# Optimization experiments

Measured on AMD Instinct MI355X. Metric: run time of the kernel, lower is better.

Reference implementation:

```python
import jax, jax.numpy as jnp
import numpy as np

B, I, H = 512, 256, 512
UNFOLDS = 6


def setup_inputs() -> dict:
    key = jax.random.key(0)
    ks = jax.random.split(key, 13)
    u = lambda k, shape, lo, hi: jax.random.uniform(k, shape, jnp.float32, lo, hi)
    sensory_erev = (2.0 * jax.random.randint(ks[3], (I, H), 0, 2) - 1.0).astype(jnp.float32)
    erev = (2.0 * jax.random.randint(ks[7], (H, H), 0, 2) - 1.0).astype(jnp.float32)
    return {
        "inputs": jax.random.normal(ks[0], (B, I), jnp.float32),
        "state": jax.random.normal(ks[1], (B, H), jnp.float32),
        "sensory_mu": u(ks[2], (I, H), 0.3, 0.8),
        "sensory_sigma": u(ks[4], (I, H), 3.0, 8.0),
        "sensory_W": u(ks[5], (I, H), 0.01, 1.0),
        "sensory_erev": sensory_erev,
        "mu": u(ks[6], (H, H), 0.3, 0.8),
        "sigma": u(ks[8], (H, H), 3.0, 8.0),
        "W": u(ks[9], (H, H), 0.01, 1.0),
        "erev": erev,
        "vleak": u(ks[10], (H,), -0.2, 0.2),
        "gleak": jnp.ones((H,), jnp.float32),
        "cm": jnp.full((H,), 0.5, jnp.float32),
    }


def reference(inputs, state, sensory_mu, sensory_sigma, sensory_W, sensory_erev,
              mu, sigma, W, erev, vleak, gleak, cm):
    # Sensory synapse currents (computed once): (B, I, H) broadcast
    sensory_act = jax.nn.sigmoid((inputs[:, :, None] - sensory_mu[None]) * sensory_sigma[None])
    sensory_w_act = sensory_W[None] * sensory_act                      # (B, I, H)
    w_num_sensory = jnp.sum(sensory_w_act * sensory_erev[None], axis=1)  # (B, H)
    w_den_sensory = jnp.sum(sensory_w_act, axis=1)                        # (B, H)

    def step(v_pre, _):
        # recurrent synapse gating: (B, H_pre, H_post)
        act = jax.nn.sigmoid((v_pre[:, :, None] - mu[None]) * sigma[None])
        w_act = W[None] * act
        w_num = jnp.sum(w_act * erev[None], axis=1) + w_num_sensory
        w_den = jnp.sum(w_act, axis=1) + w_den_sensory
        numerator = cm * v_pre + gleak * vleak + w_num
        denominator = cm + gleak + w_den
        return numerator / (denominator + 1e-8), None

    v_pre, _ = jax.lax.scan(step, state, None, length=UNFOLDS)
    return v_pre
```

## Files before the change

kernel.cpp:

```cpp
#include <hip/hip_runtime.h>

#define LTC_B 512
#define LTC_H 512
#define LTC_I 256

static constexpr float kL2E = 1.4426950408889634f;

struct alignas(16) HPair { _Float16 a0, a1, c0, c1, wz0, wz1, wd0, wd1; };

typedef unsigned int u32;
#define AS_G __attribute__((address_space(1)))
#define AS_L __attribute__((address_space(3)))

__device__ __forceinline__ void ldg_lds16(const void* g, void* l) {
    __builtin_amdgcn_global_load_lds((const AS_G u32*)g, (AS_L u32*)l, 16, 0, 0);
}

template<int K>
__global__ void ltc_prep(const float* __restrict__ mu, const float* __restrict__ sigma,
                         const float* __restrict__ W, const float* __restrict__ erev,
                         HPair* __restrict__ slab) {
    const int t = blockIdx.x * 256 + threadIdx.x;
    if (t >= K * 256) return;
    const int hh   = t & 63;
    const int rest = t >> 6;
    const int jp   = rest & (K / 2 - 1);
    const int ht   = rest / (K / 2);
    const int h    = ht * 64 + hh;
    const int g0   = (2 * jp) * LTC_H + h;
    const int g1   = g0 + LTC_H;
    HPair o;
    o.a0 = (_Float16)(-sigma[g0] * kL2E);
    o.a1 = (_Float16)(-sigma[g1] * kL2E);
    o.c0 = (_Float16)(mu[g0] * sigma[g0] * kL2E);
    o.c1 = (_Float16)(mu[g1] * sigma[g1] * kL2E);
    o.wz0 = (_Float16)(W[g0] * erev[g0]);
    o.wz1 = (_Float16)(W[g1] * erev[g1]);
    o.wd0 = (_Float16)(W[g0]);
    o.wd1 = (_Float16)(W[g1]);
    slab[t] = o;
}

template<int K, bool RECUR>
__global__ __launch_bounds__(256, 4)
void ltc_pass(const float* __restrict__ vsrc,
              const HPair* __restrict__ slab,
              const float* __restrict__ snum, const float* __restrict__ sden,
              const float* __restrict__ vleak, const float* __restrict__ gleak,
              const float* __restrict__ cm,
              float* __restrict__ onum, float* __restrict__ oden,
              float* __restrict__ vout)
{
    __shared__ HPair wbuf[2][16 * 64];
    const int tid  = threadIdx.x;
    const int lane = tid & 63;
    const int wu   = __builtin_amdgcn_readfirstlane(tid >> 6);
    const int ht   = blockIdx.x;
    const int b    = blockIdx.y * 4 + wu;
    const float* __restrict__ vrow = vsrc + (size_t)b * K;

    constexpr int NC = K / 32;
    const int rot = (int)((blockIdx.x + 7u * blockIdx.y) & (NC - 1));
    const char* slabt = (const char*)slab + (size_t)ht * (K * 512);

    {
        const char* src = slabt + rot * 16384 + wu * 4096;
        char* dst = (char*)&wbuf[0][0] + wu * 4096;
        #pragma unroll
        for (int rr = 0; rr < 4; ++rr)
            ldg_lds16(src + rr * 1024 + lane * 16, dst + rr * 1024);
    }

    float na = 0.f, da = 0.f;

    #pragma unroll
    for (int i = 0; i < NC; ++i) {
        const int c = (rot + i) & (NC - 1);
        __syncthreads();
        if (i + 1 < NC) {
            const int cn = (rot + i + 1) & (NC - 1);
            const char* src = slabt + cn * 16384 + wu * 4096;
            char* dst = (char*)&wbuf[(i + 1) & 1][0] + wu * 4096;
            #pragma unroll
            for (int rr = 0; rr < 4; ++rr)
                ldg_lds16(src + rr * 1024 + lane * 16, dst + rr * 1024);
        }
        const HPair* wb = &wbuf[i & 1][0];
        const float* __restrict__ vch = vrow + c * 32;

        HPair pr[16];
        #pragma unroll
        for (int jj = 0; jj < 16; ++jj) pr[jj] = wb[jj * 64 + lane];

        #pragma unroll
        for (int jj = 0; jj < 16; ++jj) {
            const float vj0 = vch[2 * jj];
            const float vj1 = vch[2 * jj + 1];
            const float t0 = fmaf((float)pr[jj].a0, vj0, (float)pr[jj].c0);
            const float t1 = fmaf((float)pr[jj].a1, vj1, (float)pr[jj].c1);
            const float e0 = __builtin_amdgcn_exp2f(t0);
            const float e1 = __builtin_amdgcn_exp2f(t1);
            const float d0 = 1.0f + e0;
            const float d1 = 1.0f + e1;
            const float rr = __builtin_amdgcn_rcpf(d0 * d1);
            const float s0 = rr * d1;
            const float s1 = rr * d0;
            na = fmaf((float)pr[jj].wz0, s0, na);
            da = fmaf((float)pr[jj].wd0, s0, da);
            na = fmaf((float)pr[jj].wz1, s1, na);
            da = fmaf((float)pr[jj].wd1, s1, da);
        }
    }

    const int h  = ht * 64 + lane;
    const int bh = b * LTC_H + h;
    if constexpr (RECUR) {
        const float gl = gleak[h], vl = vleak[h], c0 = cm[h];
        const float vp = vsrc[bh];
        const float num = fmaf(c0, vp, gl * vl) + na + snum[bh];
        const float den = c0 + gl + da + sden[bh];
        vout[bh] = num * __builtin_amdgcn_rcpf(den + 1e-8f);
    } else {
        onum[bh] = na;
        oden[bh] = da;
    }
}

extern "C" void kernel_launch(void* const* d_in, const int* in_sizes, int n_in,
                              void* d_out, int out_size, void* d_ws, size_t ws_size,
                              hipStream_t stream) {
    const float* inputs = (const float*)d_in[0];
    const float* state  = (const float*)d_in[1];
    const float* smu    = (const float*)d_in[2];
    const float* ssig   = (const float*)d_in[3];
    const float* sW     = (const float*)d_in[4];
    const float* serev  = (const float*)d_in[5];
    const float* mu     = (const float*)d_in[6];
    const float* sig    = (const float*)d_in[7];
    const float* W      = (const float*)d_in[8];
    const float* erev   = (const float*)d_in[9];
    const float* vleak  = (const float*)d_in[10];
    const float* gleak  = (const float*)d_in[11];
    const float* cm     = (const float*)d_in[12];

    float* out  = (float*)d_out;
    char*  ws   = (char*)d_ws;
    float* snum = (float*)(ws);
    float* sden = (float*)(ws + 1 * 1048576);
    float* vA   = (float*)(ws + 2 * 1048576);
    HPair* rslab = (HPair*)(ws + 3 * 1048576);
    HPair* sslab = (HPair*)(ws + 5 * 1048576);

    ltc_prep<LTC_H><<<LTC_H * 256 / 256, 256, 0, stream>>>(mu, sig, W, erev, rslab);
    ltc_prep<LTC_I><<<LTC_I * 256 / 256, 256, 0, stream>>>(smu, ssig, sW, serev, sslab);

    dim3 grid(LTC_H / 64, LTC_B / 4);
    dim3 blk(256);

    ltc_pass<LTC_I, false><<<grid, blk, 0, stream>>>(
        inputs, sslab, nullptr, nullptr, nullptr, nullptr, nullptr,
        snum, sden, nullptr);

    const float* vin = state;
    float* targets[6] = {vA, out, vA, out, vA, out};
    for (int s = 0; s < 6; ++s) {
        ltc_pass<LTC_H, true><<<grid, blk, 0, stream>>>(
            vin, rslab, snum, sden, vleak, gleak, cm,
            nullptr, nullptr, targets[s]);
        vin = targets[s];
    }
}
```

Baseline: 334.4 us.

## Split weight slab into fp32 gate coefficients and fp16 weights using fdot2

Splits the per-synapse slab into a float4 array of fp32 sigmoid coefficients and a separate fp16 weight pair array, each double-buffered in LDS with smaller 16-row chunks. The sigmoid pair is packed to fp16 and both accumulations use a packed fp16 dot2 instruction. The per-block chunk rotation is removed, and the previous-state load now reads from the already offset row. This cuts the fp16-to-fp32 conversions and FMA count, but raises global and LDS traffic for the coefficients and adds fp16 rounding of the activations.

Measured after the change: 346.5 us. 3.6% more time.

```diff
diff --git a/kernel.cpp b/kernel.cpp
--- a/kernel.cpp
+++ b/kernel.cpp
@@ -6,9 +6,12 @@
 
 static constexpr float kL2E = 1.4426950408889634f;
 
-struct alignas(16) HPair { _Float16 a0, a1, c0, c1, wz0, wz1, wd0, wd1; };
+typedef _Float16 half2v __attribute__((ext_vector_type(2)));
+typedef __fp16   fp16x2 __attribute__((ext_vector_type(2)));
+typedef unsigned int u32;
 
-typedef unsigned int u32;
+struct alignas(8) WPair { half2v wz, wd; };
+
 #define AS_G __attribute__((address_space(1)))
 #define AS_L __attribute__((address_space(3)))
 
@@ -19,7 +22,7 @@
 template<int K>
 __global__ void ltc_prep(const float* __restrict__ mu, const float* __restrict__ sigma,
                          const float* __restrict__ W, const float* __restrict__ erev,
-                         HPair* __restrict__ slab) {
+                         float4* __restrict__ acs, WPair* __restrict__ wps) {
     const int t = blockIdx.x * 256 + threadIdx.x;
     if (t >= K * 256) return;
     const int hh   = t & 63;
@@ -29,29 +32,33 @@
     const int h    = ht * 64 + hh;
     const int g0   = (2 * jp) * LTC_H + h;
     const int g1   = g0 + LTC_H;
-    HPair o;
-    o.a0 = (_Float16)(-sigma[g0] * kL2E);
-    o.a1 = (_Float16)(-sigma[g1] * kL2E);
-    o.c0 = (_Float16)(mu[g0] * sigma[g0] * kL2E);
-    o.c1 = (_Float16)(mu[g1] * sigma[g1] * kL2E);
-    o.wz0 = (_Float16)(W[g0] * erev[g0]);
-    o.wz1 = (_Float16)(W[g1] * erev[g1]);
-    o.wd0 = (_Float16)(W[g0]);
-    o.wd1 = (_Float16)(W[g1]);
-    slab[t] = o;
+    const float sg0 = sigma[g0], sg1 = sigma[g1];
+    acs[t] = make_float4(-sg0 * kL2E, -sg1 * kL2E,
+                         mu[g0] * sg0 * kL2E, mu[g1] * sg1 * kL2E);
+    WPair o;
+    o.wz[0] = (_Float16)(W[g0] * erev[g0]);
+    o.wz[1] = (_Float16)(W[g1] * erev[g1]);
+    o.wd[0] = (_Float16)(W[g0]);
+    o.wd[1] = (_Float16)(W[g1]);
+    wps[t] = o;
 }
 
 template<int K, bool RECUR>
 __global__ __launch_bounds__(256, 4)
 void ltc_pass(const float* __restrict__ vsrc,
-              const HPair* __restrict__ slab,
+              const float4* __restrict__ acs,
+              const WPair*  __restrict__ wps,
               const float* __restrict__ snum, const float* __restrict__ sden,
               const float* __restrict__ vleak, const float* __restrict__ gleak,
               const float* __restrict__ cm,
               float* __restrict__ onum, float* __restrict__ oden,
               float* __restrict__ vout)
 {
-    __shared__ HPair wbuf[2][16 * 64];
+    constexpr int JC = 16;
+    constexpr int PC = JC / 2;
+    constexpr int NC = K / JC;
+    __shared__ float4 acb[2][PC * 64];
+    __shared__ WPair  wpb[2][PC * 64];
     const int tid  = threadIdx.x;
     const int lane = tid & 63;
     const int wu   = __builtin_amdgcn_readfirstlane(tid >> 6);
@@ -59,45 +66,43 @@
     const int b    = blockIdx.y * 4 + wu;
     const float* __restrict__ vrow = vsrc + (size_t)b * K;
 
-    constexpr int NC = K / 32;
-    const int rot = (int)((blockIdx.x + 7u * blockIdx.y) & (NC - 1));
-    const char* slabt = (const char*)slab + (size_t)ht * (K * 512);
+    const char* acg = (const char*)acs + (size_t)ht * (K * 512);
+    const char* wpg = (const char*)wps + (size_t)ht * (K * 256);
 
     {
-        const char* src = slabt + rot * 16384 + wu * 4096;
-        char* dst = (char*)&wbuf[0][0] + wu * 4096;
-        #pragma unroll
-        for (int rr = 0; rr < 4; ++rr)
-            ldg_lds16(src + rr * 1024 + lane * 16, dst + rr * 1024);
+        char* acd = (char*)&acb[0][0];
+        char* wpd = (char*)&wpb[0][0];
+        ldg_lds16(acg + wu * 1024 + lane * 16,       acd + wu * 1024);
+        ldg_lds16(acg + (wu + 4) * 1024 + lane * 16, acd + (wu + 4) * 1024);
+        ldg_lds16(wpg + wu * 1024 + lane * 16,       wpd + wu * 1024);
     }
 
     float na = 0.f, da = 0.f;
 
     #pragma unroll
     for (int i = 0; i < NC; ++i) {
-        const int c = (rot + i) & (NC - 1);
         __syncthreads();
         if (i + 1 < NC) {
-            const int cn = (rot + i + 1) & (NC - 1);
-            const char* src = slabt + cn * 16384 + wu * 4096;
-            char* dst = (char*)&wbuf[(i + 1) & 1][0] + wu * 4096;
-            #pragma unroll
-            for (int rr = 0; rr < 4; ++rr)
-                ldg_lds16(src + rr * 1024 + lane * 16, dst + rr * 1024);
+            const char* as = acg + (i + 1) * 8192;
+            const char* ps = wpg + (i + 1) * 4096;
+            char* acd = (char*)&acb[(i + 1) & 1][0];
+            char* wpd = (char*)&wpb[(i + 1) & 1][0];
+            ldg_lds16(as + wu * 1024 + lane * 16,       acd + wu * 1024);
+            ldg_lds16(as + (wu + 4) * 1024 + lane * 16, acd + (wu + 4) * 1024);
+            ldg_lds16(ps + wu * 1024 + lane * 16,       wpd + wu * 1024);
         }
-        const HPair* wb = &wbuf[i & 1][0];
-        const float* __restrict__ vch = vrow + c * 32;
-
-        HPair pr[16];
-        #pragma unroll
-        for (int jj = 0; jj < 16; ++jj) pr[jj] = wb[jj * 64 + lane];
+        const float4* ab = &acb[i & 1][0];
+        const WPair*  pb = &wpb[i & 1][0];
+        const float* __restrict__ vch = vrow + i * JC;
 
         #pragma unroll
-        for (int jj = 0; jj < 16; ++jj) {
+        for (int jj = 0; jj < PC; ++jj) {
+            const float4 ac = ab[jj * 64 + lane];
+            const WPair  wp = pb[jj * 64 + lane];
             const float vj0 = vch[2 * jj];
             const float vj1 = vch[2 * jj + 1];
-            const float t0 = fmaf((float)pr[jj].a0, vj0, (float)pr[jj].c0);
-            const float t1 = fmaf((float)pr[jj].a1, vj1, (float)pr[jj].c1);
+            const float t0 = fmaf(ac.x, vj0, ac.z);
+            const float t1 = fmaf(ac.y, vj1, ac.w);
             const float e0 = __builtin_amdgcn_exp2f(t0);
             const float e1 = __builtin_amdgcn_exp2f(t1);
             const float d0 = 1.0f + e0;
@@ -105,10 +110,15 @@
             const float rr = __builtin_amdgcn_rcpf(d0 * d1);
             const float s0 = rr * d1;
             const float s1 = rr * d0;
-            na = fmaf((float)pr[jj].wz0, s0, na);
-            da = fmaf((float)pr[jj].wd0, s0, da);
-            na = fmaf((float)pr[jj].wz1, s1, na);
-            da = fmaf((float)pr[jj].wd1, s1, da);
+            const fp16x2 spraw = __builtin_amdgcn_cvt_pkrtz(s0, s1);
+            const half2v sp = __builtin_bit_cast(half2v, spraw);
+#if defined(__has_builtin) && __has_builtin(__builtin_amdgcn_fdot2)
+            na = __builtin_amdgcn_fdot2(wp.wz, sp, na, false);
+            da = __builtin_amdgcn_fdot2(wp.wd, sp, da, false);
+#else
+            na = fmaf((float)wp.wz[0], s0, fmaf((float)wp.wz[1], s1, na));
+            da = fmaf((float)wp.wd[0], s0, fmaf((float)wp.wd[1], s1, da));
+#endif
         }
     }
 
@@ -116,7 +126,7 @@
     const int bh = b * LTC_H + h;
     if constexpr (RECUR) {
         const float gl = gleak[h], vl = vleak[h], c0 = cm[h];
-        const float vp = vsrc[bh];
+        const float vp = vrow[h];
         const float num = fmaf(c0, vp, gl * vl) + na + snum[bh];
         const float den = c0 + gl + da + sden[bh];
         vout[bh] = num * __builtin_amdgcn_rcpf(den + 1e-8f);
@@ -145,27 +155,30 @@
 
     float* out  = (float*)d_out;
     char*  ws   = (char*)d_ws;
-    float* snum = (float*)(ws);
-    float* sden = (float*)(ws + 1 * 1048576);
-    float* vA   = (float*)(ws + 2 * 1048576);
-    HPair* rslab = (HPair*)(ws + 3 * 1048576);
-    HPair* sslab = (HPair*)(ws + 5 * 1048576);
+    const size_t MB = 1048576;
+    float*  snum  = (float*)(ws);
+    float*  sden  = (float*)(ws + 1 * MB);
+    float*  vA    = (float*)(ws + 2 * MB);
+    float4* rac   = (float4*)(ws + 3 * MB);
+    WPair*  rwp   = (WPair*) (ws + 7 * MB);
+    float4* sac   = (float4*)(ws + 9 * MB);
+    WPair*  swp   = (WPair*) (ws + 11 * MB);
 
-    ltc_prep<LTC_H><<<LTC_H * 256 / 256, 256, 0, stream>>>(mu, sig, W, erev, rslab);
-    ltc_prep<LTC_I><<<LTC_I * 256 / 256, 256, 0, stream>>>(smu, ssig, sW, serev, sslab);
+    ltc_prep<LTC_H><<<LTC_H * 256 / 256, 256, 0, stream>>>(mu, sig, W, erev, rac, rwp);
+    ltc_prep<LTC_I><<<LTC_I * 256 / 256, 256, 0, stream>>>(smu, ssig, sW, serev, sac, swp);
 
     dim3 grid(LTC_H / 64, LTC_B / 4);
     dim3 blk(256);
 
     ltc_pass<LTC_I, false><<<grid, blk, 0, stream>>>(
-        inputs, sslab, nullptr, nullptr, nullptr, nullptr, nullptr,
+        inputs, sac, swp, nullptr, nullptr, nullptr, nullptr, nullptr,
         snum, sden, nullptr);
 
     const float* vin = state;
     float* targets[6] = {vA, out, vA, out, vA, out};
     for (int s = 0; s < 6; ++s) {
         ltc_pass<LTC_H, true><<<grid, blk, 0, stream>>>(
-            vin, rslab, snum, sden, vleak, gleak, cm,
+            vin, rac, rwp, snum, sden, vleak, gleak, cm,
             nullptr, nullptr, targets[s]);
         vin = targets[s];
     }
```

## Keep synapse weights in registers, split K across waves, add fp16 dot2 accumulation

Applied to the files above, without the earlier changes.

Each wave now holds its 64-row slice of the precomputed weight slab in registers and loops over 8 batch rows, replacing per-block LDS double-buffered streaming of weights. The reduction dimension is split across the four waves and across a grid dimension, with partials reduced via LDS and written as float2 partial sums. A separate finalize kernel combines the partials with the sensory terms and computes the state update. Sigmoid outputs are packed to fp16 and accumulated with fdot2. This trades extra kernel launches, partial-sum traffic and reduced precision for weight reuse across batch rows.

Measured after the change: 405.7 us. 21.3% more time.

```diff
diff --git a/kernel.cpp b/kernel.cpp
--- a/kernel.cpp
+++ b/kernel.cpp
@@ -6,15 +6,10 @@
 
 static constexpr float kL2E = 1.4426950408889634f;
 
+typedef _Float16 half2v __attribute__((ext_vector_type(2)));
+typedef __fp16   fp16x2 __attribute__((ext_vector_type(2)));
+
 struct alignas(16) HPair { _Float16 a0, a1, c0, c1, wz0, wz1, wd0, wd1; };
-
-typedef unsigned int u32;
-#define AS_G __attribute__((address_space(1)))
-#define AS_L __attribute__((address_space(3)))
-
-__device__ __forceinline__ void ldg_lds16(const void* g, void* l) {
-    __builtin_amdgcn_global_load_lds((const AS_G u32*)g, (AS_L u32*)l, 16, 0, 0);
-}
 
 template<int K>
 __global__ void ltc_prep(const float* __restrict__ mu, const float* __restrict__ sigma,
@@ -41,89 +36,83 @@
     slab[t] = o;
 }
 
-template<int K, bool RECUR>
-__global__ __launch_bounds__(256, 4)
-void ltc_pass(const float* __restrict__ vsrc,
-              const HPair* __restrict__ slab,
-              const float* __restrict__ snum, const float* __restrict__ sden,
-              const float* __restrict__ vleak, const float* __restrict__ gleak,
-              const float* __restrict__ cm,
-              float* __restrict__ onum, float* __restrict__ oden,
-              float* __restrict__ vout)
+template<int K>
+__global__ __launch_bounds__(256, 2)
+void ltc_wpass(const float* __restrict__ vsrc,
+               const HPair* __restrict__ slab,
+               float2* __restrict__ pout)
 {
-    __shared__ HPair wbuf[2][16 * 64];
-    const int tid  = threadIdx.x;
-    const int lane = tid & 63;
-    const int wu   = __builtin_amdgcn_readfirstlane(tid >> 6);
+    __shared__ float2 cb[2][4][64];
+    const int lane = threadIdx.x & 63;
+    const int wave = threadIdx.x >> 6;
     const int ht   = blockIdx.x;
-    const int b    = blockIdx.y * 4 + wu;
-    const float* __restrict__ vrow = vsrc + (size_t)b * K;
+    const int ks   = blockIdx.y;
+    const int jb   = (ks * 4 + wave) * 64;
+    const int b0   = blockIdx.z * 8;
+    float2* __restrict__ po = pout + (size_t)ks * (LTC_B * LTC_H);
 
-    constexpr int NC = K / 32;
-    const int rot = (int)((blockIdx.x + 7u * blockIdx.y) & (NC - 1));
-    const char* slabt = (const char*)slab + (size_t)ht * (K * 512);
-
-    {
-        const char* src = slabt + rot * 16384 + wu * 4096;
-        char* dst = (char*)&wbuf[0][0] + wu * 4096;
-        #pragma unroll
-        for (int rr = 0; rr < 4; ++rr)
-            ldg_lds16(src + rr * 1024 + lane * 16, dst + rr * 1024);
+    const HPair* wsl = slab + ((size_t)ht * (K / 2) + (jb >> 1)) * 64 + lane;
+    float  wa0[32], wa1[32], wc0[32], wc1[32];
+    half2v wz[32], wd[32];
+    #pragma unroll
+    for (int p = 0; p < 32; ++p) {
+        const HPair hp = wsl[p * 64];
+        wa0[p] = (float)hp.a0;  wa1[p] = (float)hp.a1;
+        wc0[p] = (float)hp.c0;  wc1[p] = (float)hp.c1;
+        wz[p]  = half2v{hp.wz0, hp.wz1};
+        wd[p]  = half2v{hp.wd0, hp.wd1};
     }
 
-    float na = 0.f, da = 0.f;
-
-    #pragma unroll
-    for (int i = 0; i < NC; ++i) {
-        const int c = (rot + i) & (NC - 1);
-        __syncthreads();
-        if (i + 1 < NC) {
-            const int cn = (rot + i + 1) & (NC - 1);
-            const char* src = slabt + cn * 16384 + wu * 4096;
-            char* dst = (char*)&wbuf[(i + 1) & 1][0] + wu * 4096;
-            #pragma unroll
-            for (int rr = 0; rr < 4; ++rr)
-                ldg_lds16(src + rr * 1024 + lane * 16, dst + rr * 1024);
-        }
-        const HPair* wb = &wbuf[i & 1][0];
-        const float* __restrict__ vch = vrow + c * 32;
-
-        HPair pr[16];
+    for (int ib = 0; ib < 8; ++ib) {
+        const int b = b0 + ib;
+        const float* __restrict__ vb = vsrc + (size_t)b * K + jb;
+        float na = 0.f, da = 0.f;
         #pragma unroll
-        for (int jj = 0; jj < 16; ++jj) pr[jj] = wb[jj * 64 + lane];
-
-        #pragma unroll
-        for (int jj = 0; jj < 16; ++jj) {
-            const float vj0 = vch[2 * jj];
-            const float vj1 = vch[2 * jj + 1];
-            const float t0 = fmaf((float)pr[jj].a0, vj0, (float)pr[jj].c0);
-            const float t1 = fmaf((float)pr[jj].a1, vj1, (float)pr[jj].c1);
+        for (int p = 0; p < 32; ++p) {
+            const float vj0 = vb[2 * p];
+            const float vj1 = vb[2 * p + 1];
+            const float t0 = fmaf(wa0[p], vj0, wc0[p]);
+            const float t1 = fmaf(wa1[p], vj1, wc1[p]);
             const float e0 = __builtin_amdgcn_exp2f(t0);
             const float e1 = __builtin_amdgcn_exp2f(t1);
             const float d0 = 1.0f + e0;
             const float d1 = 1.0f + e1;
             const float rr = __builtin_amdgcn_rcpf(d0 * d1);
-            const float s0 = rr * d1;
-            const float s1 = rr * d0;
-            na = fmaf((float)pr[jj].wz0, s0, na);
-            da = fmaf((float)pr[jj].wd0, s0, da);
-            na = fmaf((float)pr[jj].wz1, s1, na);
-            da = fmaf((float)pr[jj].wd1, s1, da);
+            const fp16x2 spr = __builtin_amdgcn_cvt_pkrtz(rr * d1, rr * d0);
+            const half2v sp  = __builtin_bit_cast(half2v, spr);
+            na = __builtin_amdgcn_fdot2(wz[p], sp, na, false);
+            da = __builtin_amdgcn_fdot2(wd[p], sp, da, false);
+        }
+        cb[ib & 1][wave][lane] = float2{na, da};
+        __syncthreads();
+        if (wave == (ib & 3)) {
+            const float2 q0 = cb[ib & 1][0][lane];
+            const float2 q1 = cb[ib & 1][1][lane];
+            const float2 q2 = cb[ib & 1][2][lane];
+            const float2 q3 = cb[ib & 1][3][lane];
+            float2 r;
+            r.x = (q0.x + q1.x) + (q2.x + q3.x);
+            r.y = (q0.y + q1.y) + (q2.y + q3.y);
+            po[(size_t)b * LTC_H + ht * 64 + lane] = r;
         }
     }
+}
 
-    const int h  = ht * 64 + lane;
-    const int bh = b * LTC_H + h;
-    if constexpr (RECUR) {
-        const float gl = gleak[h], vl = vleak[h], c0 = cm[h];
-        const float vp = vsrc[bh];
-        const float num = fmaf(c0, vp, gl * vl) + na + snum[bh];
-        const float den = c0 + gl + da + sden[bh];
-        vout[bh] = num * __builtin_amdgcn_rcpf(den + 1e-8f);
-    } else {
-        onum[bh] = na;
-        oden[bh] = da;
-    }
+__global__ __launch_bounds__(256)
+void ltc_fin(const float* __restrict__ vpre, const float2* __restrict__ pnd,
+             const float2* __restrict__ snd,
+             const float* __restrict__ vleak, const float* __restrict__ gleak,
+             const float* __restrict__ cm, float* __restrict__ vout)
+{
+    const int i = blockIdx.x * 256 + threadIdx.x;
+    const int h = i & (LTC_H - 1);
+    const float2 p0 = pnd[i];
+    const float2 p1 = pnd[LTC_B * LTC_H + i];
+    const float2 s  = snd[i];
+    const float gl = gleak[h], c = cm[h];
+    const float num = fmaf(c, vpre[i], gl * vleak[h]) + p0.x + p1.x + s.x;
+    const float den = c + gl + p0.y + p1.y + s.y;
+    vout[i] = num * __builtin_amdgcn_rcpf(den + 1e-8f);
 }
 
 extern "C" void kernel_launch(void* const* d_in, const int* in_sizes, int n_in,
@@ -145,28 +134,25 @@
 
     float* out  = (float*)d_out;
     char*  ws   = (char*)d_ws;
-    float* snum = (float*)(ws);
-    float* sden = (float*)(ws + 1 * 1048576);
-    float* vA   = (float*)(ws + 2 * 1048576);
-    HPair* rslab = (HPair*)(ws + 3 * 1048576);
-    HPair* sslab = (HPair*)(ws + 5 * 1048576);
+    const size_t MB = 1048576;
+    float2* sND   = (float2*)(ws);
+    float2* pND   = (float2*)(ws + 2 * MB);
+    float*  vA    = (float*) (ws + 6 * MB);
+    float*  vB    = (float*) (ws + 7 * MB);
+    HPair*  rslab = (HPair*) (ws + 8 * MB);
+    HPair*  sslab = (HPair*) (ws + 10 * MB);
 
     ltc_prep<LTC_H><<<LTC_H * 256 / 256, 256, 0, stream>>>(mu, sig, W, erev, rslab);
     ltc_prep<LTC_I><<<LTC_I * 256 / 256, 256, 0, stream>>>(smu, ssig, sW, serev, sslab);
 
-    dim3 grid(LTC_H / 64, LTC_B / 4);
-    dim3 blk(256);
+    ltc_wpass<LTC_I><<<dim3(8, 1, 64), 256, 0, stream>>>(inputs, sslab, sND);
 
-    ltc_pass<LTC_I, false><<<grid, blk, 0, stream>>>(
-        inputs, sslab, nullptr, nullptr, nullptr, nullptr, nullptr,
-        snum, sden, nullptr);
-
-    const float* vin = state;
-    float* targets[6] = {vA, out, vA, out, vA, out};
+    const float* vpre = state;
+    float* vtgt[6] = {vA, vB, vA, vB, vA, out};
     for (int s = 0; s < 6; ++s) {
-        ltc_pass<LTC_H, true><<<grid, blk, 0, stream>>>(
-            vin, rslab, snum, sden, vleak, gleak, cm,
-            nullptr, nullptr, targets[s]);
-        vin = targets[s];
+        ltc_wpass<LTC_H><<<dim3(8, 2, 64), 256, 0, stream>>>(vpre, rslab, pND);
+        ltc_fin<<<LTC_B * LTC_H / 256, 256, 0, stream>>>(
+            vpre, pND, sND, vleak, gleak, cm, vtgt[s]);
+        vpre = vtgt[s];
     }
 }
```
